# Optimization experiments

Measured on AMD Instinct MI355X. Metric: run time of the kernel, lower is better.

Reference implementation:

```python
import jax, jax.numpy as jnp
import numpy as np

DEPTH = 8
IN_FEATURES = 512
OUT_FEATURES = 64
BATCH = 4096
LEAF_COUNT = 2 ** DEPTH          # 256
GATE_COUNT = LEAF_COUNT - 1      # 255


def tree_paths(depth):
    """Replicates the torch loop: for each leaf i, the gate index visited at each
    level j and whether the path takes the right branch (bit '1' -> 1-gating)."""
    leaves = 2 ** depth
    idx = np.zeros((depth, leaves), dtype=np.int32)
    bit = np.zeros((depth, leaves), dtype=bool)
    for i in range(leaves):
        bits = np.binary_repr(i, width=depth)
        index = 1
        for j in range(depth):
            idx[j, i] = index - 1
            bit[j, i] = (bits[j] == '1')
            index = 2 * index + (1 if bits[j] == '1' else 0)
    return idx, bit


def setup_inputs() -> dict:
    key = jax.random.key(0)
    kx, kg, kp = jax.random.split(key, 3)
    x = jax.random.normal(kx, (BATCH, IN_FEATURES), dtype=jnp.float32)
    # kaiming_normal_(nonlinearity='sigmoid') on [gate_count, in_features]: gain=1,
    # fan_in = in_features -> std = 1/sqrt(in_features); stored transposed.
    gw = jax.random.normal(kg, (IN_FEATURES, GATE_COUNT), dtype=jnp.float32) / np.sqrt(IN_FEATURES)
    gb = jnp.zeros((GATE_COUNT,), dtype=jnp.float32)
    # kaiming_normal_(nonlinearity='linear') on [out*leaf, in]: std = 1/sqrt(in_features),
    # reshaped to [out, leaf, in] then permuted to [out, in, leaf].
    pw = jax.random.normal(kp, (OUT_FEATURES, IN_FEATURES, LEAF_COUNT), dtype=jnp.float32) / np.sqrt(IN_FEATURES)
    pb = jnp.zeros((OUT_FEATURES, LEAF_COUNT), dtype=jnp.float32)
    idx, bit = tree_paths(DEPTH)
    return {
        'x': x, 'gw': gw, 'gb': gb, 'pw': pw, 'pb': pb,
        'leaf_idx': jnp.asarray(idx), 'leaf_bit': jnp.asarray(bit),
    }


def reference(x, gw, gb, pw, pb, leaf_idx, leaf_bit):
    # gatings: [B, gate_count]
    gatings = jax.nn.sigmoid(x @ gw + gb)
    # gather gate prob along each leaf path: [B, depth, leaf_count]
    g_sel = gatings[:, leaf_idx]
    branch = jnp.where(leaf_bit[None], 1.0 - g_sel, g_sel)
    leaf_probs = jnp.prod(branch, axis=1)            # [B, leaf_count]
    # per-leaf projection of x, plus bias: [B, out, leaf_count]
    per_leaf = jnp.einsum('bi,oil->bol', x, pw) + pb[None]
    # mixture over leaves: [B, out]
    return jnp.einsum('bol,bl->bo', per_leaf, leaf_probs)
```

## Files before the change

kernel.cpp:

```cpp
#include <hip/hip_runtime.h>
#include <cstdint>
#include <cstddef>

#define GATES 255

typedef __attribute__((ext_vector_type(8))) short bf16x8;
typedef __attribute__((ext_vector_type(4))) float f32x4;

__device__ __forceinline__ short f2bf(float f) {
  union { float f; uint32_t u; } c; c.f = f;
  uint32_t r = c.u + 0x7FFFu + ((c.u >> 16) & 1u);
  return (short)(r >> 16);
}

#define GLOAD16(gp, lp) __builtin_amdgcn_global_load_lds( \
    (const __attribute__((address_space(1))) uint32_t*)(gp), \
    (__attribute__((address_space(3))) uint32_t*)(lp), 16, 0, 0)

__global__ __launch_bounds__(256) void k_prep(const float* __restrict__ x,
                                              short* __restrict__ xb,
                                              const float* __restrict__ gw,
                                              short* __restrict__ gwt,
                                              const float* __restrict__ pw,
                                              short* __restrict__ pwt) {
  __shared__ short t[64][65];
  const int bx = blockIdx.x;
  const int tid = threadIdx.x;

  if (bx < 2048) {
    const int i = bx * 256 + tid;
    const float4 v = ((const float4*)x)[i];
    short4 s;
    s.x = f2bf(v.x); s.y = f2bf(v.y); s.z = f2bf(v.z); s.w = f2bf(v.w);
    ((short4*)xb)[i] = s;
    return;
  }

  const int c = tid & 63, r0 = tid >> 6;

  if (bx < 2080) {
    const int b2 = bx - 2048;
    const int ib = b2 >> 2, gb = b2 & 3;
    const int i0 = ib << 6, g0 = gb << 6;
#pragma unroll
    for (int rr = 0; rr < 16; ++rr) {
      const int i = rr * 4 + r0;
      const int g = g0 + c;
      t[i][c] = (g < GATES) ? f2bf(gw[(size_t)(i0 + i) * GATES + g]) : (short)0;
    }
    __syncthreads();
#pragma unroll
    for (int rr = 0; rr < 16; ++rr) {
      const int gg = rr * 4 + r0;
      gwt[(size_t)(g0 + gg) * 512 + i0 + c] = t[c][gg];
    }
    return;
  }

  const int b2 = bx - 2080;
  const int o = b2 >> 5;
  const int ib = (b2 >> 2) & 7;
  const int lb = b2 & 3;
  const int i0 = ib << 6, l0 = lb << 6;
  const float* src = pw + ((size_t)o * 512 + i0) * 256 + l0;
#pragma unroll
  for (int rr = 0; rr < 16; ++rr) {
    const int i = rr * 4 + r0;
    t[i][c] = f2bf(src[(size_t)i * 256 + c]);
  }
  __syncthreads();
  short* dst = pwt + ((size_t)o * 256 + l0) * 512 + i0;
#pragma unroll
  for (int rr = 0; rr < 16; ++rr) {
    const int ll = rr * 4 + r0;
    dst[(size_t)ll * 512 + c] = t[c][ll];
  }
}

__global__ __launch_bounds__(256, 1) void k_gate(const short* __restrict__ xb,
                                                 const short* __restrict__ gwt,
                                                 const float* __restrict__ gb,
                                                 float* __restrict__ p) {
  __shared__ short a_lds[64 * 64];
  __shared__ short b_lds[256 * 64];
  __shared__ float gs[64][260];

  const int b0 = blockIdx.x << 6;
  const int tid = threadIdx.x;
  const int lane = tid & 63;
  const int w = tid >> 6;
  const int wr = w >> 1, wc = w & 1;

  const short* Ab = xb + (size_t)b0 * 512;

  f32x4 acc[2][8];
#pragma unroll
  for (int mf = 0; mf < 2; ++mf)
#pragma unroll
    for (int nf = 0; nf < 8; ++nf) {
      acc[mf][nf][0] = 0.f; acc[mf][nf][1] = 0.f;
      acc[mf][nf][2] = 0.f; acc[mf][nf][3] = 0.f;
    }

  for (int s = 0; s < 8; ++s) {
    const int i0 = s << 6;
    __syncthreads();
#pragma unroll
    for (int sw = 0; sw < 2; ++sw) {
      const int chunk = sw * 256 + tid;
      const int r = chunk >> 3, c = (chunk & 7) << 3;
      GLOAD16(Ab + (size_t)r * 512 + i0 + c, a_lds + chunk * 8);
    }
#pragma unroll
    for (int sw = 0; sw < 8; ++sw) {
      const int chunk = sw * 256 + tid;
      const int r = chunk >> 3, c = (chunk & 7) << 3;
      GLOAD16(gwt + (size_t)r * 512 + i0 + c, b_lds + chunk * 8);
    }
    __syncthreads();
#pragma unroll
    for (int kk = 0; kk < 2; ++kk) {
      const int kb = (kk << 5) + ((lane >> 4) << 3);
      bf16x8 af[2], bfr[8];
#pragma unroll
      for (int mf = 0; mf < 2; ++mf) {
        const int row = (wr << 5) + (mf << 4) + (lane & 15);
        af[mf] = *(const bf16x8*)(a_lds + row * 64 + kb);
      }
#pragma unroll
      for (int nf = 0; nf < 8; ++nf) {
        const int row = (wc << 7) + (nf << 4) + (lane & 15);
        bfr[nf] = *(const bf16x8*)(b_lds + row * 64 + kb);
      }
#pragma unroll
      for (int mf = 0; mf < 2; ++mf)
#pragma unroll
        for (int nf = 0; nf < 8; ++nf)
          acc[mf][nf] = __builtin_amdgcn_mfma_f32_16x16x32_bf16(
              af[mf], bfr[nf], acc[mf][nf], 0, 0, 0);
    }
  }

  const int grp = lane >> 4, lcol = lane & 15;
#pragma unroll
  for (int nf = 0; nf < 8; ++nf) {
    const int g = (wc << 7) + (nf << 4) + lcol;
    const float bias = (g < GATES) ? gb[g] : 0.f;
#pragma unroll
    for (int mf = 0; mf < 2; ++mf)
#pragma unroll
      for (int rg = 0; rg < 4; ++rg) {
        const int bl = (wr << 5) + (mf << 4) + (grp << 2) + rg;
        const float z = acc[mf][nf][rg] + bias;
        gs[bl][g] = 1.f / (1.f + __expf(-z));
      }
  }
  __syncthreads();

  const int l = tid;
  for (int r = 0; r < 64; ++r) {
    float prob = 1.f;
    int index = 1;
#pragma unroll
    for (int j = 0; j < 8; ++j) {
      const int bit = (l >> (7 - j)) & 1;
      const float gg = gs[r][index - 1];
      prob *= bit ? (1.f - gg) : gg;
      index = 2 * index + bit;
    }
    p[(size_t)(b0 + r) * 256 + l] = prob;
  }
}

__global__ __launch_bounds__(256, 2) void k_main(const short* __restrict__ xb,
                                                 const short* __restrict__ pwt,
                                                 const float* __restrict__ p,
                                                 const float* __restrict__ pb,
                                                 float* __restrict__ out) {
  __shared__ short a_lds[128 * 64];
  __shared__ short b_lds[256 * 64];
  __shared__ float red[2][128];

  const int bx = blockIdx.x;
  const int o = bx >> 5;
  const int bm0 = (bx & 31) << 7;
  const int tid = threadIdx.x;
  const int lane = tid & 63;
  const int w = tid >> 6;
  const int wr = w >> 1;
  const int wc = w & 1;

  const short* Ab = xb + (size_t)bm0 * 512;
  const short* Bb = pwt + (size_t)o * (256 * 512);

  f32x4 acc[4][8];
#pragma unroll
  for (int mf = 0; mf < 4; ++mf)
#pragma unroll
    for (int nf = 0; nf < 8; ++nf) {
      acc[mf][nf][0] = 0.f; acc[mf][nf][1] = 0.f;
      acc[mf][nf][2] = 0.f; acc[mf][nf][3] = 0.f;
    }

  for (int s = 0; s < 8; ++s) {
    const int i0 = s << 6;
    __syncthreads();
#pragma unroll
    for (int sw = 0; sw < 4; ++sw) {
      const int chunk = sw * 256 + tid;
      const int r = chunk >> 3;
      const int c = (chunk & 7) << 3;
      GLOAD16(Ab + (size_t)r * 512 + i0 + c, a_lds + chunk * 8);
    }
#pragma unroll
    for (int sw = 0; sw < 8; ++sw) {
      const int chunk = sw * 256 + tid;
      const int r = chunk >> 3;
      const int c = (chunk & 7) << 3;
      GLOAD16(Bb + (size_t)r * 512 + i0 + c, b_lds + chunk * 8);
    }
    __syncthreads();
#pragma unroll
    for (int kk = 0; kk < 2; ++kk) {
      const int kb = (kk << 5) + ((lane >> 4) << 3);
      bf16x8 af[4], bfr[8];
#pragma unroll
      for (int mf = 0; mf < 4; ++mf) {
        const int row = (wr << 6) + (mf << 4) + (lane & 15);
        af[mf] = *(const bf16x8*)(a_lds + row * 64 + kb);
      }
#pragma unroll
      for (int nf = 0; nf < 8; ++nf) {
        const int row = (wc << 7) + (nf << 4) + (lane & 15);
        bfr[nf] = *(const bf16x8*)(b_lds + row * 64 + kb);
      }
#pragma unroll
      for (int mf = 0; mf < 4; ++mf)
#pragma unroll
        for (int nf = 0; nf < 8; ++nf)
          acc[mf][nf] = __builtin_amdgcn_mfma_f32_16x16x32_bf16(
              af[mf], bfr[nf], acc[mf][nf], 0, 0, 0);
    }
  }

  const int grp = lane >> 4;
  const int lcol = lane & 15;
  float pbv[8];
#pragma unroll
  for (int nf = 0; nf < 8; ++nf)
    pbv[nf] = pb[(size_t)o * 256 + (wc << 7) + (nf << 4) + lcol];
#pragma unroll
  for (int mf = 0; mf < 4; ++mf) {
#pragma unroll
    for (int rg = 0; rg < 4; ++rg) {
      const int bl = (wr << 6) + (mf << 4) + (grp << 2) + rg;
      const int b = bm0 + bl;
      float v = 0.f;
#pragma unroll
      for (int nf = 0; nf < 8; ++nf) {
        const int l = (wc << 7) + (nf << 4) + lcol;
        v += (acc[mf][nf][rg] + pbv[nf]) * p[(size_t)b * 256 + l];
      }
      v += __shfl_xor(v, 1);
      v += __shfl_xor(v, 2);
      v += __shfl_xor(v, 4);
      v += __shfl_xor(v, 8);
      if (lcol == 0) red[wc][bl] = v;
    }
  }
  __syncthreads();
  if (tid < 128) {
    out[(size_t)(bm0 + tid) * 64 + o] = red[0][tid] + red[1][tid];
  }
}

extern "C" void kernel_launch(void* const* d_in, const int* in_sizes, int n_in,
                              void* d_out, int out_size, void* d_ws, size_t ws_size,
                              hipStream_t stream) {
  (void)in_sizes; (void)n_in; (void)out_size; (void)ws_size;
  const float* x  = (const float*)d_in[0];
  const float* gw = (const float*)d_in[1];
  const float* gb = (const float*)d_in[2];
  const float* pw = (const float*)d_in[3];
  const float* pb = (const float*)d_in[4];
  float* out = (float*)d_out;

  char* ws = (char*)d_ws;
  short* xbuf = (short*)(ws);
  short* gwt  = (short*)(ws + ((size_t)4 << 20));
  short* pwt  = (short*)(ws + ((size_t)4 << 20) + (256 << 10));
  float* p    = (float*)(ws + ((size_t)20 << 20) + (256 << 10));

  k_prep<<<4128, 256, 0, stream>>>(x, xbuf, gw, gwt, pw, pwt);
  k_gate<<<64, 256, 0, stream>>>(xbuf, gwt, gb, p);
  k_main<<<2048, 256, 0, stream>>>(xbuf, pwt, p, pb, out);
}
```

Before: 135.7 us.

## Double-buffer LDS, swizzle layout, and enlarge main GEMM tile to 256x256

The main mixture GEMM now uses 512-thread blocks, each computing a 256-batch by 256-leaf tile for one output feature. The LDS buffers are double-buffered so the next K-slice's global_load_lds is issued before computing the current slice, with one barrier per step. An XOR swizzle on 16-byte blocks is added to cut LDS bank conflicts on the fragment reads. The cost is 128KB of LDS and one block per CU, which limits occupancy and latency hiding across blocks.

```diff
diff --git a/kernel.cpp b/kernel.cpp
--- a/kernel.cpp
+++ b/kernel.cpp
@@ -172,105 +172,118 @@
   }
 }
 
-__global__ __launch_bounds__(256, 2) void k_main(const short* __restrict__ xb,
+__global__ __launch_bounds__(512, 1) void k_main(const short* __restrict__ xb,
                                                  const short* __restrict__ pwt,
                                                  const float* __restrict__ p,
                                                  const float* __restrict__ pb,
                                                  float* __restrict__ out) {
-  __shared__ short a_lds[128 * 64];
-  __shared__ short b_lds[256 * 64];
-  __shared__ float red[2][128];
+  __shared__ short lds[2][2][256 * 64];
 
   const int bx = blockIdx.x;
-  const int o = bx >> 5;
-  const int bm0 = (bx & 31) << 7;
+  const int o = bx >> 4;
+  const int bm0 = (bx & 15) << 8;
   const int tid = threadIdx.x;
   const int lane = tid & 63;
   const int w = tid >> 6;
-  const int wr = w >> 1;
-  const int wc = w & 1;
+  const int wr = w >> 2;
+  const int wc = w & 3;
 
   const short* Ab = xb + (size_t)bm0 * 512;
   const short* Bb = pwt + (size_t)o * (256 * 512);
 
-  f32x4 acc[4][8];
-#pragma unroll
-  for (int mf = 0; mf < 4; ++mf)
-#pragma unroll
-    for (int nf = 0; nf < 8; ++nf) {
+  f32x4 acc[8][4];
+#pragma unroll
+  for (int mf = 0; mf < 8; ++mf)
+#pragma unroll
+    for (int nf = 0; nf < 4; ++nf) {
       acc[mf][nf][0] = 0.f; acc[mf][nf][1] = 0.f;
       acc[mf][nf][2] = 0.f; acc[mf][nf][3] = 0.f;
     }
 
-  for (int s = 0; s < 8; ++s) {
-    const int i0 = s << 6;
-    __syncthreads();
-#pragma unroll
-    for (int sw = 0; sw < 4; ++sw) {
-      const int chunk = sw * 256 + tid;
-      const int r = chunk >> 3;
-      const int c = (chunk & 7) << 3;
-      GLOAD16(Ab + (size_t)r * 512 + i0 + c, a_lds + chunk * 8);
-    }
-#pragma unroll
-    for (int sw = 0; sw < 8; ++sw) {
-      const int chunk = sw * 256 + tid;
-      const int r = chunk >> 3;
-      const int c = (chunk & 7) << 3;
-      GLOAD16(Bb + (size_t)r * 512 + i0 + c, b_lds + chunk * 8);
-    }
-    __syncthreads();
+  auto stage = [&](int buf, int t) {
+    const int i0 = t << 6;
+#pragma unroll
+    for (int j = 0; j < 4; ++j) {
+      const int c = j * 512 + tid;
+      const int r = c >> 3;
+      const int blk = (c & 7) ^ (r & 7);
+      GLOAD16(Ab + (size_t)r * 512 + i0 + (blk << 3), &lds[buf][0][c * 8]);
+    }
+#pragma unroll
+    for (int j = 0; j < 4; ++j) {
+      const int c = j * 512 + tid;
+      const int r = c >> 3;
+      const int blk = (c & 7) ^ (r & 7);
+      GLOAD16(Bb + (size_t)r * 512 + i0 + (blk << 3), &lds[buf][1][c * 8]);
+    }
+  };
+
+  auto compute = [&](int buf) {
 #pragma unroll
     for (int kk = 0; kk < 2; ++kk) {
-      const int kb = (kk << 5) + ((lane >> 4) << 3);
-      bf16x8 af[4], bfr[8];
-#pragma unroll
-      for (int mf = 0; mf < 4; ++mf) {
-        const int row = (wr << 6) + (mf << 4) + (lane & 15);
-        af[mf] = *(const bf16x8*)(a_lds + row * 64 + kb);
-      }
-#pragma unroll
-      for (int nf = 0; nf < 8; ++nf) {
-        const int row = (wc << 7) + (nf << 4) + (lane & 15);
-        bfr[nf] = *(const bf16x8*)(b_lds + row * 64 + kb);
-      }
-#pragma unroll
-      for (int mf = 0; mf < 4; ++mf)
-#pragma unroll
-        for (int nf = 0; nf < 8; ++nf)
+      const int blkcol = (kk << 2) + (lane >> 4);
+      bf16x8 af[8], bfr[4];
+#pragma unroll
+      for (int nf = 0; nf < 4; ++nf) {
+        const int row = (wc << 6) + (nf << 4) + (lane & 15);
+        const int blk = blkcol ^ (row & 7);
+        bfr[nf] = *(const bf16x8*)(&lds[buf][1][row * 64 + (blk << 3)]);
+      }
+#pragma unroll
+      for (int mf = 0; mf < 8; ++mf) {
+        const int row = (wr << 7) + (mf << 4) + (lane & 15);
+        const int blk = blkcol ^ (row & 7);
+        af[mf] = *(const bf16x8*)(&lds[buf][0][row * 64 + (blk << 3)]);
+      }
+#pragma unroll
+      for (int mf = 0; mf < 8; ++mf)
+#pragma unroll
+        for (int nf = 0; nf < 4; ++nf)
           acc[mf][nf] = __builtin_amdgcn_mfma_f32_16x16x32_bf16(
               af[mf], bfr[nf], acc[mf][nf], 0, 0, 0);
     }
-  }
-
+  };
+
+  stage(0, 0);
+  __syncthreads();
+  for (int t = 0; t < 7; ++t) {
+    stage((t + 1) & 1, t + 1);
+    compute(t & 1);
+    __syncthreads();
+  }
+  compute(1);
+  __syncthreads();
+
+  float* red = (float*)&lds[0][0][0];
   const int grp = lane >> 4;
   const int lcol = lane & 15;
-  float pbv[8];
-#pragma unroll
-  for (int nf = 0; nf < 8; ++nf)
-    pbv[nf] = pb[(size_t)o * 256 + (wc << 7) + (nf << 4) + lcol];
-#pragma unroll
-  for (int mf = 0; mf < 4; ++mf) {
+  float pbv[4];
+#pragma unroll
+  for (int nf = 0; nf < 4; ++nf)
+    pbv[nf] = pb[(size_t)o * 256 + (wc << 6) + (nf << 4) + lcol];
+#pragma unroll
+  for (int mf = 0; mf < 8; ++mf) {
 #pragma unroll
     for (int rg = 0; rg < 4; ++rg) {
-      const int bl = (wr << 6) + (mf << 4) + (grp << 2) + rg;
+      const int bl = (wr << 7) + (mf << 4) + (grp << 2) + rg;
       const int b = bm0 + bl;
       float v = 0.f;
 #pragma unroll
-      for (int nf = 0; nf < 8; ++nf) {
-        const int l = (wc << 7) + (nf << 4) + lcol;
+      for (int nf = 0; nf < 4; ++nf) {
+        const int l = (wc << 6) + (nf << 4) + lcol;
         v += (acc[mf][nf][rg] + pbv[nf]) * p[(size_t)b * 256 + l];
       }
       v += __shfl_xor(v, 1);
       v += __shfl_xor(v, 2);
       v += __shfl_xor(v, 4);
       v += __shfl_xor(v, 8);
-      if (lcol == 0) red[wc][bl] = v;
-    }
-  }
-  __syncthreads();
-  if (tid < 128) {
-    out[(size_t)(bm0 + tid) * 64 + o] = red[0][tid] + red[1][tid];
+      if (lcol == 0) red[wc * 256 + bl] = v;
+    }
+  }
+  __syncthreads();
+  if (tid < 256) {
+    out[(size_t)(bm0 + tid) * 64 + o] =
+        red[tid] + red[256 + tid] + red[512 + tid] + red[768 + tid];
   }
 }
 
@@ -293,5 +306,5 @@
 
   k_prep<<<4128, 256, 0, stream>>>(x, xbuf, gw, gwt, pw, pwt);
   k_gate<<<64, 256, 0, stream>>>(xbuf, gwt, gb, p);
-  k_main<<<2048, 256, 0, stream>>>(xbuf, pwt, p, pb, out);
-}
+  k_main<<<1024, 512, 0, stream>>>(xbuf, pwt, p, pb, out);
+}
```

Measured after the change: 146.0 us. +7.6%, slower.
